# Kernel tuning notes

Hardware: AMD Instinct MI355X
Metric: run time of the kernel (lower is better)

The kernel has to match this reference:

```python
import jax, jax.numpy as jnp
import numpy as np

B, S = 1, 8192
QC = 4096          # query_channels
H = 64             # num_heads (== key_channels == output_channels, forced by forward body)
KC = 64            # key_channels
OC = 64            # output_channels
P = 0.25           # dropout prob


def setup_inputs() -> dict:
    key = jax.random.key(0)
    ks = jax.random.split(key, 8)
    w = lambda k, shape: jax.random.normal(k, shape, dtype=jnp.float32) * 0.02
    return {
        "query": jax.random.normal(ks[0], (B, S, QC), dtype=jnp.float32),
        "key_in": jax.random.normal(ks[1], (B, S, KC), dtype=jnp.float32),
        "value": jax.random.normal(ks[2], (B, S, KC), dtype=jnp.float32),
        "mask_u": jax.random.uniform(ks[3], (B, S, H, H), dtype=jnp.float32),
        # Linear weights stored (in, out); torch stores (out, in) but math is identical.
        "Wq": w(ks[4], (QC, H * KC)), "bq": jnp.zeros((H * KC,), jnp.float32),
        "Wk": w(ks[5], (KC, H * KC)), "bk": jnp.zeros((H * KC,), jnp.float32),
        "Wv": w(ks[6], (KC, H * OC)), "bv": jnp.zeros((H * OC,), jnp.float32),
        "Wo": w(ks[7], (H * OC, OC)), "bo": jnp.zeros((OC,), jnp.float32),
    }


def reference(query, key_in, value, mask_u, Wq, bq, Wk, bk, Wv, bv, Wo, bo):
    # Projections
    q = (query @ Wq + bq).reshape(B, S, H, KC)
    k = (key_in @ Wk + bk).reshape(B, S, H, KC)
    v = (value @ Wv + bv).reshape(B, S, H, KC)   # source views v with key_channels (Oc==Kc)
    # transpose(-2, -1): (B, S, KC, H)
    qT = jnp.swapaxes(q, -2, -1)
    kT = jnp.swapaxes(k, -2, -1)
    vT = jnp.swapaxes(v, -2, -1)
    # Per-token 'attention': contracts H of qT against KC of kT (H == KC). No sqrt(d) scale.
    attn_logits = jnp.matmul(qT, kT)             # (B, S, H, H)
    # safe_logsoftmax: numerically stable log-softmax (NOT softmax) over last dim
    attn = jax.nn.log_softmax(attn_logits, axis=-1)
    # dropout p=0.25, deterministic via precomputed uniforms
    keep = (mask_u > P).astype(attn.dtype) / (1.0 - P)
    attn = attn * keep
    out = jnp.matmul(attn, vT)                   # (B, S, H, H)
    # transpose(0,1) -> (S, B, H, H), then view(S, -1) -> (S, B*H*H) with B==1
    out = jnp.swapaxes(out, 0, 1).reshape(S, -1)
    return out @ Wo + bo                          # (S, OC)
```

## Files before the change

### kernel.cpp

```cpp
#include <hip/hip_runtime.h>
#include <stdint.h>
#include <stddef.h>

typedef unsigned short u16;
typedef __bf16 bf16x8 __attribute__((ext_vector_type(8)));
typedef float f32x4 __attribute__((ext_vector_type(4)));

#define DEVINL __device__ __forceinline__

DEVINL u16 f2bf(float f) {
  uint32_t u = __builtin_bit_cast(uint32_t, f);
  u += 0x7FFFu + ((u >> 16) & 1u);
  return (u16)(u >> 16);
}
DEVINL float bf2f(u16 h) {
  uint32_t u = ((uint32_t)h) << 16;
  return __builtin_bit_cast(float, u);
}
DEVINL uint32_t pack2(float a, float b) {
  return (uint32_t)f2bf(a) | ((uint32_t)f2bf(b) << 16);
}

DEVINL void gload_lds16(const u16* g, u16* lds) {
  __builtin_amdgcn_global_load_lds(
      (const __attribute__((address_space(1))) uint32_t*)g,
      (__attribute__((address_space(3))) uint32_t*)lds, 16, 0, 0);
}

__global__ __launch_bounds__(256) void cast_kernel(const float* __restrict__ x,
                                                   u16* __restrict__ y, int n8) {
  int i = blockIdx.x * 256 + threadIdx.x;
  if (i >= n8) return;
  const float4* xp = (const float4*)x + (size_t)i * 2;
  float4 a = xp[0], b = xp[1];
  uint4 o;
  o.x = pack2(a.x, a.y);
  o.y = pack2(a.z, a.w);
  o.z = pack2(b.x, b.y);
  o.w = pack2(b.z, b.w);
  ((uint4*)y)[i] = o;
}

__global__ __launch_bounds__(256) void transpose_cast(const float* __restrict__ W,
                                                      u16* __restrict__ Bt,
                                                      int K, int N) {
  __shared__ float tile[64][65];
  const int nb = blockIdx.x << 6, kb = blockIdx.y << 6;
  const int t = threadIdx.x;
  {
    const int kr = t >> 2, n0 = (t & 3) << 4;
    const float* src = W + (size_t)(kb + kr) * N + nb + n0;
#pragma unroll
    for (int i = 0; i < 16; i += 4) {
      float4 v = *(const float4*)(src + i);
      tile[n0 + i + 0][kr] = v.x;
      tile[n0 + i + 1][kr] = v.y;
      tile[n0 + i + 2][kr] = v.z;
      tile[n0 + i + 3][kr] = v.w;
    }
  }
  __syncthreads();
  {
    const int nr = t >> 2, k0 = (t & 3) << 4;
    u16* dst = Bt + (size_t)(nb + nr) * K + kb + k0;
#pragma unroll
    for (int i = 0; i < 16; i += 8) {
      uint4 o;
      o.x = pack2(tile[nr][k0 + i + 0], tile[nr][k0 + i + 1]);
      o.y = pack2(tile[nr][k0 + i + 2], tile[nr][k0 + i + 3]);
      o.z = pack2(tile[nr][k0 + i + 4], tile[nr][k0 + i + 5]);
      o.w = pack2(tile[nr][k0 + i + 6], tile[nr][k0 + i + 7]);
      *(uint4*)(dst + i) = o;
    }
  }
}

template <int BM, int BN, int WM, int WN, bool OUTF32, bool SPLITK>
__global__ __launch_bounds__(256) void gemm_bf16t(const u16* __restrict__ A,
                                                  const u16* __restrict__ Bt,
                                                  const float* __restrict__ bias,
                                                  void* __restrict__ Cv,
                                                  int M, int N, int K,
                                                  int lda, int ldb) {
  static_assert(WM * WN == 4, "4 waves");
  constexpr int BK = 32;
  constexpr int FM = BM / (WM * 16);
  constexpr int FN = BN / (WN * 16);
  __shared__ __align__(16) u16 Al[BM * BK];
  __shared__ __align__(16) u16 Bl[BN * BK];
  const int t = threadIdx.x;
  const int lane = t & 63, w = t >> 6;
  const int wm = w / WN, wn = w % WN;

  int bx, by;
  {
    const int nwg = gridDim.x * gridDim.y;
    int bid = blockIdx.y * gridDim.x + blockIdx.x;
    if ((nwg & 7) == 0) {
      const int cpx = nwg >> 3;
      bid = (bid & 7) * cpx + (bid >> 3);
    }
    bx = bid % gridDim.x;
    by = bid / gridDim.x;
  }

  int bn;
  float* Cpart = nullptr;
  if (SPLITK) {
    const int chunk = bx;
    A  += (size_t)chunk * K;
    Bt += (size_t)chunk * K;
    Cpart = (float*)Cv + (size_t)chunk * M * N;
    bn = 0;
  } else {
    bn = bx * BN;
  }
  const int bm = by * BM;
  const int r16 = lane & 15, khi = lane >> 4;

  f32x4 acc[FM][FN] = {};

  const int srow = t >> 2;
  const int skel = (t & 3) << 3;

  for (int k0 = 0; k0 < K; k0 += BK) {
#pragma unroll
    for (int r = 0; r < BM / 64; ++r) {
      const u16* g = A + (size_t)(bm + r * 64 + srow) * lda + k0 + skel;
      gload_lds16(g, Al + r * 2048 + (w << 9));
    }
#pragma unroll
    for (int r = 0; r < BN / 64; ++r) {
      const u16* g = Bt + (size_t)(bn + r * 64 + srow) * ldb + k0 + skel;
      gload_lds16(g, Bl + r * 2048 + (w << 9));
    }
    __syncthreads();

    bf16x8 af[FM], bfr[FN];
#pragma unroll
    for (int mi = 0; mi < FM; ++mi)
      af[mi] = *(const bf16x8*)(Al + (wm * FM * 16 + mi * 16 + r16) * BK + khi * 8);
#pragma unroll
    for (int ni = 0; ni < FN; ++ni)
      bfr[ni] = *(const bf16x8*)(Bl + (wn * FN * 16 + ni * 16 + r16) * BK + khi * 8);
#pragma unroll
    for (int mi = 0; mi < FM; ++mi)
#pragma unroll
      for (int ni = 0; ni < FN; ++ni)
        acc[mi][ni] = __builtin_amdgcn_mfma_f32_16x16x32_bf16(af[mi], bfr[ni],
                                                              acc[mi][ni], 0, 0, 0);
    __syncthreads();
  }

  const int crow0 = bm + wm * FM * 16 + (khi << 2);
  const int ccol0 = bn + wn * FN * 16 + r16;
#pragma unroll
  for (int mi = 0; mi < FM; ++mi) {
#pragma unroll
    for (int ni = 0; ni < FN; ++ni) {
      const int col = ccol0 + ni * 16;
      const float bv = (!SPLITK && bias) ? bias[col] : 0.0f;
#pragma unroll
      for (int e = 0; e < 4; ++e) {
        const int row = crow0 + mi * 16 + e;
        const float v = acc[mi][ni][e] + bv;
        if (SPLITK)
          Cpart[(size_t)row * N + col] = v;
        else if (OUTF32)
          ((float*)Cv)[(size_t)row * N + col] = v;
        else
          ((u16*)Cv)[(size_t)row * N + col] = f2bf(v);
      }
    }
  }
}

__global__ __launch_bounds__(256) void reduce_splitk(const float* __restrict__ part,
                                                     const float* __restrict__ bo,
                                                     float* __restrict__ out, int n) {
  int i = blockIdx.x * 256 + threadIdx.x;
  if (i >= n) return;
  float s = 0.0f;
#pragma unroll
  for (int c = 0; c < 8; ++c) s += part[(size_t)c * 524288 + i];
  out[i] = s + bo[i & 63];
}

__global__ __launch_bounds__(256) void attn_mfma(const u16* __restrict__ Q,
                                                 const u16* __restrict__ Kp,
                                                 const u16* __restrict__ Vp,
                                                 const float* __restrict__ mask,
                                                 u16* __restrict__ OUT) {
  constexpr int LDP = 72;
  __shared__ __align__(16) u16 Pbuf[4][64 * LDP];
  const int t = threadIdx.x;
  const int w = t >> 6, lane = t & 63;
  const int r16 = lane & 15, khi = lane >> 4;
  const int s = blockIdx.x * 4 + w;
  const size_t base = (size_t)s << 12;
  u16* pb = Pbuf[w];

  {
    uint4 rowv[8];
    const uint4* qp = (const uint4*)(Q + base + (size_t)lane * 64);
#pragma unroll
    for (int i = 0; i < 8; ++i) rowv[i] = qp[i];
#pragma unroll
    for (int i = 0; i < 8; ++i) {
      const uint32_t* wp = (const uint32_t*)&rowv[i];
#pragma unroll
      for (int h = 0; h < 4; ++h) {
        uint32_t v = wp[h];
        pb[(8 * i + 2 * h) * LDP + lane] = (u16)(v & 0xffffu);
        pb[(8 * i + 2 * h + 1) * LDP + lane] = (u16)(v >> 16);
      }
    }
  }
  asm volatile("s_waitcnt lgkmcnt(0)" ::: "memory");

  f32x4 acc[4][4] = {};
#pragma unroll
  for (int ks = 0; ks < 2; ++ks) {
    bf16x8 af[4], bfr[4];
#pragma unroll
    for (int mi = 0; mi < 4; ++mi)
      af[mi] = *(const bf16x8*)(pb + (16 * mi + r16) * LDP + ks * 32 + khi * 8);
#pragma unroll
    for (int ni = 0; ni < 4; ++ni)
      bfr[ni] = *(const bf16x8*)(Kp + base + (size_t)(16 * ni + r16) * 64 +
                                 ks * 32 + khi * 8);
#pragma unroll
    for (int mi = 0; mi < 4; ++mi)
#pragma unroll
      for (int ni = 0; ni < 4; ++ni)
        acc[mi][ni] = __builtin_amdgcn_mfma_f32_16x16x32_bf16(af[mi], bfr[ni],
                                                              acc[mi][ni], 0, 0, 0);
  }

  float L[4][4];
#pragma unroll
  for (int mi = 0; mi < 4; ++mi) {
#pragma unroll
    for (int e = 0; e < 4; ++e) {
      float mx = fmaxf(fmaxf(acc[mi][0][e], acc[mi][1][e]),
                       fmaxf(acc[mi][2][e], acc[mi][3][e]));
      mx = fmaxf(mx, __shfl_xor(mx, 1));
      mx = fmaxf(mx, __shfl_xor(mx, 2));
      mx = fmaxf(mx, __shfl_xor(mx, 4));
      mx = fmaxf(mx, __shfl_xor(mx, 8));
      float sm = __expf(acc[mi][0][e] - mx) + __expf(acc[mi][1][e] - mx) +
                 __expf(acc[mi][2][e] - mx) + __expf(acc[mi][3][e] - mx);
      sm += __shfl_xor(sm, 1);
      sm += __shfl_xor(sm, 2);
      sm += __shfl_xor(sm, 4);
      sm += __shfl_xor(sm, 8);
      L[mi][e] = mx + __logf(sm);
    }
  }

  const float* mrow = mask + base;
#pragma unroll
  for (int mi = 0; mi < 4; ++mi) {
#pragma unroll
    for (int ni = 0; ni < 4; ++ni) {
#pragma unroll
      for (int e = 0; e < 4; ++e) {
        const int c = 16 * mi + 4 * khi + e;
        const int j = 16 * ni + r16;
        const float keep = mrow[(size_t)c * 64 + j] > 0.25f ? (1.0f / 0.75f) : 0.0f;
        pb[c * LDP + j] = f2bf((acc[mi][ni][e] - L[mi][e]) * keep);
      }
    }
  }
  asm volatile("s_waitcnt lgkmcnt(0)" ::: "memory");

  f32x4 o[4][4] = {};
#pragma unroll
  for (int ks = 0; ks < 2; ++ks) {
    bf16x8 af[4], bfr[4];
#pragma unroll
    for (int mi = 0; mi < 4; ++mi)
      af[mi] = *(const bf16x8*)(pb + (16 * mi + r16) * LDP + ks * 32 + khi * 8);
#pragma unroll
    for (int ni = 0; ni < 4; ++ni)
      bfr[ni] = *(const bf16x8*)(Vp + base + (size_t)(16 * ni + r16) * 64 +
                                 ks * 32 + khi * 8);
#pragma unroll
    for (int mi = 0; mi < 4; ++mi)
#pragma unroll
      for (int ni = 0; ni < 4; ++ni)
        o[mi][ni] = __builtin_amdgcn_mfma_f32_16x16x32_bf16(af[mi], bfr[ni],
                                                            o[mi][ni], 0, 0, 0);
  }

#pragma unroll
  for (int mi = 0; mi < 4; ++mi) {
#pragma unroll
    for (int ni = 0; ni < 4; ++ni) {
#pragma unroll
      for (int e = 0; e < 4; ++e) {
        const int c = 16 * mi + 4 * khi + e;
        const int jo = 16 * ni + r16;
        OUT[base + (size_t)c * 64 + jo] = f2bf(o[mi][ni][e]);
      }
    }
  }
}

extern "C" void kernel_launch(void* const* d_in, const int* in_sizes, int n_in,
                              void* d_out, int out_size, void* d_ws, size_t ws_size,
                              hipStream_t stream) {
  (void)in_sizes; (void)n_in; (void)out_size; (void)ws_size;
  const float* query  = (const float*)d_in[0];
  const float* key_in = (const float*)d_in[1];
  const float* value  = (const float*)d_in[2];
  const float* mask_u = (const float*)d_in[3];
  const float* Wq = (const float*)d_in[4];
  const float* bq = (const float*)d_in[5];
  const float* Wk = (const float*)d_in[6];
  const float* bk = (const float*)d_in[7];
  const float* Wv = (const float*)d_in[8];
  const float* bv = (const float*)d_in[9];
  const float* Wo = (const float*)d_in[10];
  const float* bo = (const float*)d_in[11];

  char* ws = (char*)d_ws;
  u16* q_bf   = (u16*)(ws + 0);
  u16* WqT    = (u16*)(ws + ((size_t)64 << 20));
  u16* key_bf = (u16*)(ws + ((size_t)96 << 20));
  u16* val_bf = (u16*)(ws + ((size_t)97 << 20));
  u16* WkT    = (u16*)(ws + ((size_t)98 << 20));
  u16* WvT    = (u16*)(ws + ((size_t)98 << 20) + (512 << 10));
  u16* WoT    = (u16*)(ws + ((size_t)99 << 20));
  u16* Qp     = (u16*)(ws + ((size_t)100 << 20));
  u16* Kp     = (u16*)(ws + ((size_t)164 << 20));
  u16* Vp     = (u16*)(ws + ((size_t)228 << 20));
  u16* OUTb   = q_bf;
  float* part = (float*)Kp;

  cast_kernel<<<16384, 256, 0, stream>>>(query, q_bf, 8192 * 4096 / 8);
  cast_kernel<<<256, 256, 0, stream>>>(key_in, key_bf, 8192 * 64 / 8);
  cast_kernel<<<256, 256, 0, stream>>>(value, val_bf, 8192 * 64 / 8);
  transpose_cast<<<dim3(64, 64), 256, 0, stream>>>(Wq, WqT, 4096, 4096);
  transpose_cast<<<dim3(64, 1), 256, 0, stream>>>(Wk, WkT, 64, 4096);
  transpose_cast<<<dim3(64, 1), 256, 0, stream>>>(Wv, WvT, 64, 4096);
  transpose_cast<<<dim3(1, 64), 256, 0, stream>>>(Wo, WoT, 4096, 64);

  gemm_bf16t<128, 128, 2, 2, false, false>
      <<<dim3(32, 64), 256, 0, stream>>>(q_bf, WqT, bq, Qp, 8192, 4096, 4096, 4096, 4096);
  gemm_bf16t<128, 128, 2, 2, false, false>
      <<<dim3(32, 64), 256, 0, stream>>>(key_bf, WkT, bk, Kp, 8192, 4096, 64, 64, 64);
  gemm_bf16t<128, 128, 2, 2, false, false>
      <<<dim3(32, 64), 256, 0, stream>>>(val_bf, WvT, bv, Vp, 8192, 4096, 64, 64, 64);

  attn_mfma<<<2048, 256, 0, stream>>>(Qp, Kp, Vp, mask_u, OUTb);

  gemm_bf16t<128, 64, 4, 1, true, true>
      <<<dim3(8, 64), 256, 0, stream>>>(OUTb, WoT, nullptr, part, 8192, 64, 512, 4096, 4096);
  reduce_splitk<<<2048, 256, 0, stream>>>(part, bo, (float*)d_out, 8192 * 64);
}
```

Before: 865.6 us.

## Add 256x256 pipelined bf16 GEMM with swizzled LDS for Q projection

Adds a new 512-thread GEMM kernel that uses 256x256 output tiles, BK=64, and double-buffered LDS holding 128 KB. It streams the next tile's global-to-LDS loads one quarter-step at a time, interleaved with MFMA work, and uses an XOR-swizzled LDS layout to avoid bank conflicts. The large Q projection (8192x4096x4096) now uses this kernel. The generic GEMM loses its workgroup-ID remapping for L2 locality, which may change cache behaviour for the remaining small GEMMs. The big tile raises register and LDS use and cuts occupancy in exchange for more data reuse.

```diff
diff --git a/kernel.cpp b/kernel.cpp
--- a/kernel.cpp
+++ b/kernel.cpp
@@ -92,30 +92,18 @@
   const int lane = t & 63, w = t >> 6;
   const int wm = w / WN, wn = w % WN;
 
-  int bx, by;
-  {
-    const int nwg = gridDim.x * gridDim.y;
-    int bid = blockIdx.y * gridDim.x + blockIdx.x;
-    if ((nwg & 7) == 0) {
-      const int cpx = nwg >> 3;
-      bid = (bid & 7) * cpx + (bid >> 3);
-    }
-    bx = bid % gridDim.x;
-    by = bid / gridDim.x;
-  }
-
   int bn;
   float* Cpart = nullptr;
   if (SPLITK) {
-    const int chunk = bx;
+    const int chunk = blockIdx.x;
     A  += (size_t)chunk * K;
     Bt += (size_t)chunk * K;
     Cpart = (float*)Cv + (size_t)chunk * M * N;
     bn = 0;
   } else {
-    bn = bx * BN;
-  }
-  const int bm = by * BM;
+    bn = blockIdx.x * BN;
+  }
+  const int bm = blockIdx.y * BM;
   const int r16 = lane & 15, khi = lane >> 4;
 
   f32x4 acc[FM][FN] = {};
@@ -171,6 +159,109 @@
         else
           ((u16*)Cv)[(size_t)row * N + col] = f2bf(v);
       }
+    }
+  }
+}
+
+__global__ __launch_bounds__(512, 2) void gemm256(const u16* __restrict__ A,
+                                                  const u16* __restrict__ Bt,
+                                                  const float* __restrict__ bias,
+                                                  u16* __restrict__ C,
+                                                  int M, int N, int K) {
+  __shared__ __align__(16) u16 LDSu[65536];
+  const int t = threadIdx.x;
+  const int lane = t & 63, w = t >> 6;
+  const int wm = w >> 2, wn = w & 3;
+  const int r16 = lane & 15, khi = lane >> 4;
+  const int bm = blockIdx.y << 8, bn = blockIdx.x << 8;
+  const int nt = K >> 6;
+
+  const int srow = t >> 3;
+  const int scb = ((((t & 7) << 4) ^ (((t >> 3) & 7) << 4)) >> 1);
+
+  auto ISSUE_HALF = [&](int m_) {
+    const int tile_ = m_ >> 2, h_ = m_ & 3;
+    const int k0_ = tile_ << 6;
+    u16* lb_ = LDSu + ((tile_ & 1) << 15) + ((h_ & 2) << 13) + ((h_ & 1) << 13)
+               + t * 8;
+    const int row0_ = ((h_ & 1) << 7) + srow;
+    if (h_ < 2) {
+      gload_lds16(A + (size_t)(bm + row0_) * K + k0_ + scb, lb_);
+      gload_lds16(A + (size_t)(bm + row0_ + 64) * K + k0_ + scb, lb_ + 4096);
+    } else {
+      gload_lds16(Bt + (size_t)(bn + row0_) * K + k0_ + scb, lb_);
+      gload_lds16(Bt + (size_t)(bn + row0_ + 64) * K + k0_ + scb, lb_ + 4096);
+    }
+  };
+
+  f32x4 acc[8][4] = {};
+  bf16x8 bf[4][2];
+
+  for (int m = 0; m < 5; ++m) ISSUE_HALF(m);
+  asm volatile("s_waitcnt vmcnt(2)" ::: "memory");
+  __builtin_amdgcn_s_barrier();
+
+  for (int n = 0; n < nt; ++n) {
+    const u16* bufb = LDSu + ((n & 1) << 15);
+#pragma unroll
+    for (int q = 0; q < 4; ++q) {
+      bf16x8 af[2][2];
+      if (q == 0) {
+#pragma unroll
+        for (int ni = 0; ni < 4; ++ni)
+#pragma unroll
+          for (int ks = 0; ks < 2; ++ks)
+            bf[ni][ks] = *(const bf16x8*)(bufb + 16384 +
+                (64 * wn + 16 * ni + r16) * 64 +
+                ((((ks << 6) + (khi << 4)) ^ ((r16 & 7) << 4)) >> 1));
+      }
+#pragma unroll
+      for (int mi2 = 0; mi2 < 2; ++mi2)
+#pragma unroll
+        for (int ks = 0; ks < 2; ++ks)
+          af[mi2][ks] = *(const bf16x8*)(bufb +
+              (32 * (2 * q + mi2) + 16 * wm + r16) * 64 +
+              ((((ks << 6) + (khi << 4)) ^ ((r16 & 7) << 4)) >> 1));
+      __builtin_amdgcn_sched_barrier(0);
+      {
+        const int m = 4 * n + q + 5;
+        if (m < 4 * nt) ISSUE_HALF(m);
+      }
+      __builtin_amdgcn_sched_barrier(0);
+      __builtin_amdgcn_s_barrier();
+      asm volatile("s_waitcnt lgkmcnt(0)" ::: "memory");
+      __builtin_amdgcn_sched_barrier(0);
+      __builtin_amdgcn_s_setprio(1);
+#pragma unroll
+      for (int mi2 = 0; mi2 < 2; ++mi2)
+#pragma unroll
+        for (int ni = 0; ni < 4; ++ni)
+#pragma unroll
+          for (int ks = 0; ks < 2; ++ks)
+            acc[2 * q + mi2][ni] = __builtin_amdgcn_mfma_f32_16x16x32_bf16(
+                af[mi2][ks], bf[ni][ks], acc[2 * q + mi2][ni], 0, 0, 0);
+      __builtin_amdgcn_s_setprio(0);
+      __builtin_amdgcn_sched_barrier(0);
+      if (q == 3) {
+        if (n < nt - 2)
+          asm volatile("s_waitcnt vmcnt(2)" ::: "memory");
+        else
+          asm volatile("s_waitcnt vmcnt(0)" ::: "memory");
+      }
+      __builtin_amdgcn_s_barrier();
+    }
+  }
+
+#pragma unroll
+  for (int mi = 0; mi < 8; ++mi) {
+    const int row = bm + 32 * mi + 16 * wm + (khi << 2);
+#pragma unroll
+    for (int ni = 0; ni < 4; ++ni) {
+      const int col = bn + 64 * wn + 16 * ni + r16;
+      const float bv = bias[col];
+#pragma unroll
+      for (int e = 0; e < 4; ++e)
+        C[(size_t)(row + e) * N + col] = f2bf(acc[mi][ni][e] + bv);
     }
   }
 }
@@ -346,8 +437,7 @@
   transpose_cast<<<dim3(64, 1), 256, 0, stream>>>(Wv, WvT, 64, 4096);
   transpose_cast<<<dim3(1, 64), 256, 0, stream>>>(Wo, WoT, 4096, 64);
 
-  gemm_bf16t<128, 128, 2, 2, false, false>
-      <<<dim3(32, 64), 256, 0, stream>>>(q_bf, WqT, bq, Qp, 8192, 4096, 4096, 4096, 4096);
+  gemm256<<<dim3(16, 32), 512, 0, stream>>>(q_bf, WqT, bq, Qp, 8192, 4096, 4096);
   gemm_bf16t<128, 128, 2, 2, false, false>
       <<<dim3(32, 64), 256, 0, stream>>>(key_bf, WkT, bk, Kp, 8192, 4096, 64, 64, 64);
   gemm_bf16t<128, 128, 2, 2, false, false>
```

After: 708.8 us. -18.1%, faster.
